# Kernel tuning notes

Hardware: AMD Instinct MI355X
Metric: run time of the kernel (lower is better)

Reference implementation:

```python
import jax, jax.numpy as jnp
import numpy as np

B, N, H, V, STEP = 16, 50, 128, 40000, 2

def setup_inputs() -> dict:
    key = jax.random.key(0)
    ks = jax.random.split(key, 24)
    def nrm(i, shape, s=0.08):
        return jax.random.normal(ks[i], shape, jnp.float32) * s
    items = jax.random.randint(ks[0], (B, N), 0, V)
    A = jax.random.uniform(ks[1], (B, N, 2 * N), jnp.float32)
    lengths = jax.random.randint(ks[2], (B,), 1, N + 1)
    mask = (jnp.arange(N)[None, :] < lengths[:, None]).astype(jnp.int32)
    emb = nrm(3, (V, H), 0.1).at[0].set(0.0)  # padding_idx=0 row zeroed
    return dict(
        items=items, A=A, mask=mask, emb=emb,
        w_ih=nrm(4, (3 * H, 2 * H)), w_hh=nrm(5, (3 * H, H)),
        b_ih=nrm(6, (3 * H,)), b_hh=nrm(7, (3 * H,)),
        b_iah=nrm(8, (H,)), b_oah=nrm(9, (H,)),
        W_ein=nrm(10, (H, H)), b_ein=nrm(11, (H,)),
        W_eout=nrm(12, (H, H)), b_eout=nrm(13, (H,)),
        W_one=nrm(14, (H, H)), b_one=nrm(15, (H,)),
        W_two=nrm(16, (H, H)), b_two=nrm(17, (H,)),
        w_three=nrm(18, (H,)),
        W_tr=nrm(19, (H, 2 * H)), b_tr=nrm(20, (H,)),
        W_t=nrm(21, (H, H)),
    )

def gnn_cell(A, hidden, w_ih, w_hh, b_ih, b_hh, b_iah, b_oah, W_ein, b_ein, W_eout, b_eout):
    # A: [B,N,2N], hidden: [B,N,H]
    ein = hidden @ W_ein.T + b_ein
    eout = hidden @ W_eout.T + b_eout
    input_in = jnp.einsum('bnm,bmh->bnh', A[:, :, :N], ein) + b_iah
    input_out = jnp.einsum('bnm,bmh->bnh', A[:, :, N:], eout) + b_oah
    inputs = jnp.concatenate([input_in, input_out], axis=-1)  # [B,N,2H]
    gi = inputs @ w_ih.T + b_ih
    gh = hidden @ w_hh.T + b_hh
    i_r, i_i, i_n = jnp.split(gi, 3, axis=-1)
    h_r, h_i, h_n = jnp.split(gh, 3, axis=-1)
    resetgate = jax.nn.sigmoid(i_r + h_r)
    inputgate = jax.nn.sigmoid(i_i + h_i)
    newgate = jnp.tanh(i_n + resetgate * h_n)
    return newgate + inputgate * (hidden - newgate)

def reference(items, A, mask, emb, w_ih, w_hh, b_ih, b_hh, b_iah, b_oah,
              W_ein, b_ein, W_eout, b_eout, W_one, b_one, W_two, b_two,
              w_three, W_tr, b_tr, W_t):
    hidden = emb[items]  # [B,N,H]
    for _ in range(STEP):
        hidden = gnn_cell(A, hidden, w_ih, w_hh, b_ih, b_hh, b_iah, b_oah,
                          W_ein, b_ein, W_eout, b_eout)
    # compute_scores
    lengths = jnp.sum(mask, axis=1)  # all >= 1 by construction
    ht = hidden[jnp.arange(B), lengths - 1]  # [B,H] last valid item
    q1 = (ht @ W_one.T + b_one)[:, None, :]
    q2 = hidden @ W_two.T + b_two
    mexp = mask[..., None].astype(jnp.float32)  # [B,N,1]
    alpha_logits = jax.nn.sigmoid(q1 + q2) @ w_three[:, None]  # [B,N,1]
    alpha = jax.nn.softmax(jnp.where(mexp == 0, -jnp.inf, alpha_logits), axis=1)
    a = jnp.sum(alpha * hidden * mexp, axis=1)  # [B,H]
    a = jnp.concatenate([a, ht], axis=1) @ W_tr.T + b_tr  # hybrid (nonhybrid=False)
    b_emb = emb[1:]  # [V-1,H]
    qt = (hidden * mexp) @ W_t.T  # [B,N,H]
    beta_logits = jnp.einsum('vh,bnh->bvn', b_emb, qt)
    beta_logits = jnp.where(mask[:, None, :] == 0, -jnp.inf, beta_logits)
    beta = jax.nn.softmax(beta_logits, axis=-1)  # [B,V-1,N]
    target = jnp.einsum('bvn,bnh->bvh', beta, qt * mexp)  # [B,V-1,H]
    # scores = sum((a[:,None,:] + target) * b_emb, -1), split to avoid extra buffer
    scores = jnp.einsum('bvh,vh->bv', target, b_emb) + a @ b_emb.T
    return scores  # [B, V-1]
```

## Files before the change

kernel.cpp:

```cpp
#include <hip/hip_runtime.h>

#define BB 16
#define NN 50
#define HH 128
#define VV 40000
#define VO 39999

typedef unsigned short u16;
typedef unsigned int u32;
typedef __attribute__((ext_vector_type(8))) short short8;
typedef __attribute__((ext_vector_type(4))) float f32x4;

#define OFF_HID    0
#define OFF_HID2   102400
#define OFF_Q2     102400
#define OFF_Q1     204800
#define OFF_HT     206848
#define OFF_QTBF   307200
#define OFF_LEN    411648
#define OFF_WIHT   411664
#define OFF_WHHT   509968
#define OFF_WEINT  559120
#define OFF_WEOUTT 575504
#define OFF_WTWOT  591888
#define OFF_WTT    608272
#define OFF_WONET  624656
#define OFF_WTRT   641040

__device__ __forceinline__ float sigm(float x){ return 1.0f/(1.0f+__expf(-x)); }
__device__ __forceinline__ float b2f(u16 u){
  union { u32 i; float f; } c; c.i = ((u32)u) << 16; return c.f;
}
__device__ __forceinline__ u16 f2b(float f){
  union { float f; u32 i; } c; c.f = f;
  u32 u = c.i;
  return (u16)((u + 0x7fffu + ((u >> 16) & 1u)) >> 16);
}
__device__ __forceinline__ int frag_idx(int b, int n, int k){
  int tile = n>>4, vlo = n&15, kc = k>>5, quad = (k>>3)&3, j = k&7;
  return (((b*4+tile)*4+kc)<<9) + ((quad<<4)+vlo)*8 + j;
}

__global__ void k_pre(const int* __restrict__ items, const float* __restrict__ emb,
                      const float* __restrict__ w_ih, const float* __restrict__ w_hh,
                      const float* __restrict__ W_ein, const float* __restrict__ W_eout,
                      const float* __restrict__ W_two, const float* __restrict__ W_t,
                      const float* __restrict__ W_one, const float* __restrict__ W_tr,
                      float* __restrict__ ws){
  int idx = blockIdx.x*256 + threadIdx.x;
  if (idx < 102400){
    int r = idx >> 7, h = idx & 127;
    ws[OFF_HID + idx] = emb[items[r]*128 + h];
  } else if (idx < 200704){
    int i = idx-102400; int k=i/384, j=i-k*384;
    ws[OFF_WIHT + i] = w_ih[j*256 + k];
  } else if (idx < 249856){
    int i = idx-200704; int k=i/384, j=i-k*384;
    ws[OFF_WHHT + i] = w_hh[j*128 + k];
  } else if (idx < 266240){
    int i = idx-249856; int k=i>>7, h=i&127;
    ws[OFF_WEINT + i] = W_ein[h*128 + k];
  } else if (idx < 282624){
    int i = idx-266240; int k=i>>7, h=i&127;
    ws[OFF_WEOUTT + i] = W_eout[h*128 + k];
  } else if (idx < 299008){
    int i = idx-282624; int k=i>>7, h=i&127;
    ws[OFF_WTWOT + i] = W_two[h*128 + k];
  } else if (idx < 315392){
    int i = idx-299008; int k=i>>7, h=i&127;
    ws[OFF_WTT + i] = W_t[h*128 + k];
  } else if (idx < 331776){
    int i = idx-315392; int k=i>>7, h=i&127;
    ws[OFF_WONET + i] = W_one[h*128 + k];
  } else if (idx < 364544){
    int i = idx-331776; int k=i>>7, h=i&127;
    ws[OFF_WTRT + i] = W_tr[h*256 + k];
  }
}

__global__ void __launch_bounds__(384) k_step(const float* __restrict__ A,
                       const float* __restrict__ b_ein, const float* __restrict__ b_eout,
                       const float* __restrict__ b_iah, const float* __restrict__ b_oah,
                       const float* __restrict__ b_ih, const float* __restrict__ b_hh,
                       float* __restrict__ ws, int srcOff, int dstOff){
  __shared__ float hall[52][128];
  __shared__ float arow[4][104];
  __shared__ float hAl[4][256];
  __shared__ float sAl[4][2];
  __shared__ float inp[4][256];
  __shared__ float gil[4][384];
  __shared__ float ghl[4][384];
  int t = threadIdx.x;
  int tile = blockIdx.x, b = blockIdx.y;
  int n0 = tile*4;
  const float* hsrc = ws + srcOff + b*6400;
  for (int o=t; o<6656; o+=384) hall[o>>7][o&127] = (o<6400) ? hsrc[o] : 0.0f;
  for (int o=t; o<416; o+=384){
    int r=o/104, c=o-r*104;
    arow[r][c] = (c<100 && n0+r<NN) ? A[(size_t)(b*NN+n0+r)*100 + c] : 0.0f;
  }
  __syncthreads();
  for (int o=t; o<1024; o+=384){
    int r = o>>8, kk = o&255;
    int k = kk & 127;
    const float* ar = &arow[r][(kk>>7)*50];
    float acc = 0.0f;
    #pragma unroll 5
    for (int m=0;m<50;m++) acc += ar[m]*hall[m][k];
    hAl[r][kk] = acc;
  }
  if (t < 8){
    int r = t>>1, half = t&1;
    const float* ar = &arow[r][half*50];
    float s = 0.0f;
    for (int m=0;m<50;m++) s += ar[m];
    sAl[r][half] = s;
  }
  __syncthreads();
  for (int o=t; o<1024; o+=384){
    int r = o>>8, c8 = o&255;
    int in_half = (c8 < 128);
    int c = c8 & 127;
    const float* wT = ws + (in_half ? OFF_WEINT : OFF_WEOUTT);
    const float* hv = &hAl[r][in_half ? 0 : 128];
    float acc = in_half ? (b_iah[c] + sAl[r][0]*b_ein[c])
                        : (b_oah[c] + sAl[r][1]*b_eout[c]);
    for (int k=0;k<128;k+=4){
      float4 h4 = *(const float4*)(hv + k);
      acc += h4.x*wT[(k+0)*128+c] + h4.y*wT[(k+1)*128+c]
           + h4.z*wT[(k+2)*128+c] + h4.w*wT[(k+3)*128+c];
    }
    inp[r][c8] = acc;
  }
  __syncthreads();
  {
    int j = t;
    float gi[4], gh[4];
    float bi2 = b_ih[j], bh2 = b_hh[j];
    #pragma unroll
    for (int r=0;r<4;r++){ gi[r]=bi2; gh[r]=bh2; }
    const float* wti = ws + OFF_WIHT;
    const float* wth = ws + OFF_WHHT;
    for (int k=0;k<256;k+=4){
      float w0 = wti[(k+0)*384+j], w1 = wti[(k+1)*384+j];
      float w2 = wti[(k+2)*384+j], w3_ = wti[(k+3)*384+j];
      #pragma unroll
      for (int r=0;r<4;r++){
        float4 iv = *(const float4*)(&inp[r][k]);
        gi[r] += iv.x*w0 + iv.y*w1 + iv.z*w2 + iv.w*w3_;
      }
    }
    for (int k=0;k<128;k+=4){
      float w0 = wth[(k+0)*384+j], w1 = wth[(k+1)*384+j];
      float w2 = wth[(k+2)*384+j], w3_ = wth[(k+3)*384+j];
      #pragma unroll
      for (int r=0;r<4;r++){
        float4 hv = *(const float4*)(&hall[n0+r][k]);
        gh[r] += hv.x*w0 + hv.y*w1 + hv.z*w2 + hv.w*w3_;
      }
    }
    #pragma unroll
    for (int r=0;r<4;r++){ gil[r][j]=gi[r]; ghl[r][j]=gh[r]; }
  }
  __syncthreads();
  for (int o=t; o<512; o+=384){
    int r=o>>7, h=o&127, row=n0+r;
    if (row<NN){
      float ir_=gil[r][h], ii=gil[r][128+h], inw=gil[r][256+h];
      float hr_=ghl[r][h], hi2=ghl[r][128+h], hn=ghl[r][256+h];
      float rg=sigm(ir_+hr_), ig=sigm(ii+hi2), ng=tanhf(inw+rg*hn);
      float hv=hall[n0+r][h];
      ws[dstOff + (b*NN+row)*128 + h] = ng + ig*(hv-ng);
    }
  }
}

__global__ void __launch_bounds__(256) k_post(const int* __restrict__ mask,
                      const float* __restrict__ b_two, const float* __restrict__ b_one,
                      float* __restrict__ ws){
  int bx = blockIdx.x, t = threadIdx.x;
  u16* qtbf = (u16*)(ws + OFF_QTBF);
  if (bx < 200){
    bool isq2 = bx < 100;
    int r0 = (isq2 ? bx : bx-100) * 8;
    __shared__ float hl[1024];
    for (int i=0;i<4;i++) hl[t+i*256] = ws[OFF_HID + r0*128 + t + i*256];
    __syncthreads();
    int h = t & 127, g = t >> 7;
    const float* wT = ws + (isq2 ? OFF_WTWOT : OFF_WTT);
    float binit = isq2 ? b_two[h] : 0.0f;
    float acc[4];
    #pragma unroll
    for (int r=0;r<4;r++) acc[r] = binit;
    for (int k4=0;k4<32;k4++){
      int k = k4*4;
      float w0 = wT[(k+0)*128+h], w1 = wT[(k+1)*128+h];
      float w2 = wT[(k+2)*128+h], w3 = wT[(k+3)*128+h];
      #pragma unroll
      for (int r=0;r<4;r++){
        float4 hv = *(const float4*)(hl + (g*4+r)*128 + k);
        acc[r] += hv.x*w0 + hv.y*w1 + hv.z*w2 + hv.w*w3;
      }
    }
    #pragma unroll
    for (int r=0;r<4;r++){
      int row = r0 + g*4 + r;
      if (isq2) ws[OFF_Q2 + row*128 + h] = acc[r];
      else {
        float val = mask[row] ? acc[r] : 0.0f;
        int b = row/NN, n = row - b*NN;
        qtbf[frag_idx(b, n, h)] = f2b(val);
      }
    }
  } else if (bx < 248){
    int i = (bx-200)*256 + t;
    #pragma unroll
    for (int kk=0;kk<2;kk++){
      int e = i*2 + kk;
      int b = e/1536, rem = e - b*1536;
      int kc = rem/384, rem2 = rem - kc*384;
      int quad = rem2/96, vv = rem2 - quad*96;
      int vlo = 4 + vv/8, j = vv & 7;
      qtbf[(((b*4+3)*4+kc)<<9) + ((quad<<4)+vlo)*8 + j] = 0;
    }
  } else {
    __shared__ float htl[128];
    int b = bx - 248;
    if (t < 128){
      int len = 0;
      for (int n=0;n<NN;n++) len += mask[b*NN+n];
      if (len<1) len=1; if (len>NN) len=NN;
      float ht = ws[OFF_HID + (b*NN + len-1)*128 + t];
      ws[OFF_HT + b*128 + t] = ht;
      htl[t] = ht;
      if (t==0) ((int*)(ws+OFF_LEN))[b] = len;
    }
    __syncthreads();
    if (t < 128){
      const float* w1T = ws + OFF_WONET;
      float q1 = b_one[t];
      for (int k=0;k<128;k+=4){
        float4 h4 = *(const float4*)(htl + k);
        q1 += h4.x*w1T[(k+0)*128+t] + h4.y*w1T[(k+1)*128+t]
            + h4.z*w1T[(k+2)*128+t] + h4.w*w1T[(k+3)*128+t];
      }
      ws[OFF_Q1 + b*128 + t] = q1;
    }
  }
}

__global__ void __launch_bounds__(256) k_attn2(const float* __restrict__ w_three,
                        const float* __restrict__ b_tr, float* __restrict__ ws){
  __shared__ float q2l[NN*129];
  __shared__ float q1l[128], w3l[128], htl[128], al[128], pt2[128], alg[64];
  int t = threadIdx.x;
  int b = blockIdx.x;
  for (int o=t;o<6400;o+=256){ int n=o>>7, h=o&127; q2l[n*129+h] = ws[OFF_Q2 + b*6400 + o]; }
  if (t < 128){
    q1l[t] = ws[OFF_Q1 + b*128 + t];
    w3l[t] = w_three[t];
    htl[t] = ws[OFF_HT + b*128 + t];
  }
  int len = ((const int*)(ws+OFF_LEN))[b];
  __syncthreads();
  if (t < 200){
    int n = t>>2, part = t&3;
    if (n < len){
      const float* qr  = q2l + n*129 + part*32;
      const float* q1p = q1l + part*32;
      const float* w3p = w3l + part*32;
      float s = 0.0f;
      for (int h=0;h<32;h++) s += w3p[h]*sigm(q1p[h]+qr[h]);
      s += __shfl_xor(s,1); s += __shfl_xor(s,2);
      if (part==0) alg[n] = s;
    }
  }
  __syncthreads();
  if (t < 64){
    float v = (t<len) ? alg[t] : -1e30f;
    float m = v;
    m = fmaxf(m, __shfl_xor(m,1));  m = fmaxf(m, __shfl_xor(m,2));
    m = fmaxf(m, __shfl_xor(m,4));  m = fmaxf(m, __shfl_xor(m,8));
    m = fmaxf(m, __shfl_xor(m,16)); m = fmaxf(m, __shfl_xor(m,32));
    float e = (t<len) ? __expf(v - m) : 0.0f;
    float ss = e;
    ss += __shfl_xor(ss,1);  ss += __shfl_xor(ss,2);
    ss += __shfl_xor(ss,4);  ss += __shfl_xor(ss,8);
    ss += __shfl_xor(ss,16); ss += __shfl_xor(ss,32);
    float inv = 1.0f/ss;
    if (t<len) alg[t] = e*inv;
  }
  __syncthreads();
  if (t < 128){
    const float* hid = ws + OFF_HID + b*6400;
    float a = 0.0f;
    for (int n=0;n<len;n++) a += alg[n]*hid[n*128+t];
    al[t] = a;
  }
  __syncthreads();
  float p1 = 0.0f;
  if (t < 256){
    int g2 = t>>7, h = t&127;
    const float* wtr = ws + OFF_WTRT + g2*128*128;
    const float* src = g2 ? htl : al;
    float p = 0.0f;
    for (int k=0;k<128;k++) p += src[k]*wtr[k*128+h];
    if (g2) pt2[h] = p; else p1 = p;
  }
  __syncthreads();
  if (t < 128){
    float af = b_tr[t] + p1 + pt2[t];
    u16 hi = f2b(af);
    u16 lo = f2b(af - b2f(hi));
    u16* qtbf = (u16*)(ws + OFF_QTBF);
    qtbf[frag_idx(b, 50, t)] = hi;
    qtbf[frag_idx(b, 51, t)] = lo;
  }
}

__global__ void __launch_bounds__(256) k_scores(const float* __restrict__ emb,
                                                const float* __restrict__ ws,
                                                float* __restrict__ out){
  __shared__ u16 qlds[8192];
  int tid = threadIdx.x;
  int lane = tid & 63, wave = tid >> 6;
  int quad = lane >> 4, vlo = lane & 15;
  int v = blockIdx.y*64 + wave*16 + vlo;
  int vc = (v < VO) ? v : (VO-1);
  const float* erow = emb + (size_t)(vc+1)*128;
  short8 bfr[4];
  #pragma unroll
  for (int kc=0;kc<4;kc++){
    const float4* p = (const float4*)(erow + kc*32 + quad*8);
    float4 x = p[0], y = p[1];
    union { short8 s; u32 w[4]; } u;
    u.w[0] = (u32)f2b(x.x) | ((u32)f2b(x.y)<<16);
    u.w[1] = (u32)f2b(x.z) | ((u32)f2b(x.w)<<16);
    u.w[2] = (u32)f2b(y.x) | ((u32)f2b(y.y)<<16);
    u.w[3] = (u32)f2b(y.z) | ((u32)f2b(y.w)<<16);
    bfr[kc] = u.s;
  }
  const u16* qtf = (const u16*)(ws + OFF_QTBF);
  const int* slen = (const int*)(ws + OFF_LEN);
  int b0 = blockIdx.x*4;
  for (int bi=0;bi<4;bi++){
    int b = b0 + bi;
    __syncthreads();
    {
      const uint4* src = (const uint4*)qtf + (size_t)b*1024;
      uint4* dst = (uint4*)qlds;
      #pragma unroll
      for (int r=0;r<4;r++) dst[tid + r*256] = src[tid + r*256];
    }
    __syncthreads();
    int len = slen[b];
    f32x4 acc0={0.f,0.f,0.f,0.f}, acc1=acc0, acc2=acc0, acc3=acc0;
    #pragma unroll
    for (int kc=0;kc<4;kc++){
      const u16* base = qlds + kc*512 + lane*8;
      short8 a0 = *(const short8*)(base + 0*2048);
      short8 a1 = *(const short8*)(base + 1*2048);
      short8 a2 = *(const short8*)(base + 2*2048);
      short8 a3 = *(const short8*)(base + 3*2048);
      acc0 = __builtin_amdgcn_mfma_f32_16x16x32_bf16(a0, bfr[kc], acc0, 0,0,0);
      acc1 = __builtin_amdgcn_mfma_f32_16x16x32_bf16(a1, bfr[kc], acc1, 0,0,0);
      acc2 = __builtin_amdgcn_mfma_f32_16x16x32_bf16(a2, bfr[kc], acc2, 0,0,0);
      acc3 = __builtin_amdgcn_mfma_f32_16x16x32_bf16(a3, bfr[kc], acc3, 0,0,0);
    }
    int nb = quad*4;
    float ss=0.f, nm=0.f;
    #pragma unroll
    for (int r=0;r<4;r++){
      { int n=nb+r;    if(n<len){ float e=__expf(acc0[r]); ss+=e; nm+=e*acc0[r]; } }
      { int n=nb+r+16; if(n<len){ float e=__expf(acc1[r]); ss+=e; nm+=e*acc1[r]; } }
      { int n=nb+r+32; if(n<len){ float e=__expf(acc2[r]); ss+=e; nm+=e*acc2[r]; } }
      { int n=nb+r+48; if(n<len){ float e=__expf(acc3[r]); ss+=e; nm+=e*acc3[r]; } }
    }
    ss += __shfl_xor(ss,16); ss += __shfl_xor(ss,32);
    nm += __shfl_xor(nm,16); nm += __shfl_xor(nm,32);
    if (quad==0 && v < VO){
      float pa = acc3[2] + acc3[3];
      out[(size_t)b*VO + v] = nm/ss + pa;
    }
  }
}

extern "C" void kernel_launch(void* const* d_in, const int* in_sizes, int n_in,
                              void* d_out, int out_size, void* d_ws, size_t ws_size,
                              hipStream_t stream){
  const int*   items  = (const int*)d_in[0];
  const float* A      = (const float*)d_in[1];
  const int*   mask   = (const int*)d_in[2];
  const float* emb    = (const float*)d_in[3];
  const float* w_ih   = (const float*)d_in[4];
  const float* w_hh   = (const float*)d_in[5];
  const float* b_ih   = (const float*)d_in[6];
  const float* b_hh   = (const float*)d_in[7];
  const float* b_iah  = (const float*)d_in[8];
  const float* b_oah  = (const float*)d_in[9];
  const float* W_ein  = (const float*)d_in[10];
  const float* b_ein  = (const float*)d_in[11];
  const float* W_eout = (const float*)d_in[12];
  const float* b_eout = (const float*)d_in[13];
  const float* W_one  = (const float*)d_in[14];
  const float* b_one  = (const float*)d_in[15];
  const float* W_two  = (const float*)d_in[16];
  const float* b_two  = (const float*)d_in[17];
  const float* w_three= (const float*)d_in[18];
  const float* W_tr   = (const float*)d_in[19];
  const float* b_tr   = (const float*)d_in[20];
  const float* W_t    = (const float*)d_in[21];
  float* ws  = (float*)d_ws;
  float* out = (float*)d_out;

  k_pre<<<1424,256,0,stream>>>(items,emb,w_ih,w_hh,W_ein,W_eout,W_two,W_t,W_one,W_tr,ws);
  k_step<<<dim3(13,16),384,0,stream>>>(A,b_ein,b_eout,b_iah,b_oah,b_ih,b_hh,ws,OFF_HID,OFF_HID2);
  k_step<<<dim3(13,16),384,0,stream>>>(A,b_ein,b_eout,b_iah,b_oah,b_ih,b_hh,ws,OFF_HID2,OFF_HID);
  k_post<<<264,256,0,stream>>>(mask,b_two,b_one,ws);
  k_attn2<<<16,256,0,stream>>>(w_three,b_tr,ws);
  k_scores<<<dim3(4,625),256,0,stream>>>(emb,ws,out);
}
```

Before: 213.9 us.

## Read GNN weights row-major directly and halve rows per k_step block

Removes the transposed copies of w_ih, w_hh, W_ein and W_eout from the preprocessing kernel. k_step now reads the original row-major weights with per-thread float4 loads along k. Each block handles 2 node rows instead of 4, so the grid grows from 13x16 to 25x16 blocks. The aim is to cut preprocessing work and raise parallelism in the recurrent step. The cost is that each thread now walks its own weight row, so adjacent threads are strided apart and loads are uncoalesced, and every weight is re-read by twice as many blocks.

```diff
diff --git a/kernel.cpp b/kernel.cpp
--- a/kernel.cpp
+++ b/kernel.cpp
@@ -18,10 +18,6 @@
 #define OFF_HT     206848
 #define OFF_QTBF   307200
 #define OFF_LEN    411648
-#define OFF_WIHT   411664
-#define OFF_WHHT   509968
-#define OFF_WEINT  559120
-#define OFF_WEOUTT 575504
 #define OFF_WTWOT  591888
 #define OFF_WTT    608272
 #define OFF_WONET  624656
@@ -42,8 +38,6 @@
 }
 
 __global__ void k_pre(const int* __restrict__ items, const float* __restrict__ emb,
-                      const float* __restrict__ w_ih, const float* __restrict__ w_hh,
-                      const float* __restrict__ W_ein, const float* __restrict__ W_eout,
                       const float* __restrict__ W_two, const float* __restrict__ W_t,
                       const float* __restrict__ W_one, const float* __restrict__ W_tr,
                       float* __restrict__ ws){
@@ -51,56 +45,46 @@
   if (idx < 102400){
     int r = idx >> 7, h = idx & 127;
     ws[OFF_HID + idx] = emb[items[r]*128 + h];
-  } else if (idx < 200704){
-    int i = idx-102400; int k=i/384, j=i-k*384;
-    ws[OFF_WIHT + i] = w_ih[j*256 + k];
-  } else if (idx < 249856){
-    int i = idx-200704; int k=i/384, j=i-k*384;
-    ws[OFF_WHHT + i] = w_hh[j*128 + k];
-  } else if (idx < 266240){
-    int i = idx-249856; int k=i>>7, h=i&127;
-    ws[OFF_WEINT + i] = W_ein[h*128 + k];
-  } else if (idx < 282624){
-    int i = idx-266240; int k=i>>7, h=i&127;
-    ws[OFF_WEOUTT + i] = W_eout[h*128 + k];
-  } else if (idx < 299008){
-    int i = idx-282624; int k=i>>7, h=i&127;
+  } else if (idx < 118784){
+    int i = idx-102400; int k=i>>7, h=i&127;
     ws[OFF_WTWOT + i] = W_two[h*128 + k];
-  } else if (idx < 315392){
-    int i = idx-299008; int k=i>>7, h=i&127;
+  } else if (idx < 135168){
+    int i = idx-118784; int k=i>>7, h=i&127;
     ws[OFF_WTT + i] = W_t[h*128 + k];
-  } else if (idx < 331776){
-    int i = idx-315392; int k=i>>7, h=i&127;
+  } else if (idx < 151552){
+    int i = idx-135168; int k=i>>7, h=i&127;
     ws[OFF_WONET + i] = W_one[h*128 + k];
-  } else if (idx < 364544){
-    int i = idx-331776; int k=i>>7, h=i&127;
+  } else if (idx < 184320){
+    int i = idx-151552; int k=i>>7, h=i&127;
     ws[OFF_WTRT + i] = W_tr[h*256 + k];
   }
 }
 
 __global__ void __launch_bounds__(384) k_step(const float* __restrict__ A,
+                       const float* __restrict__ w_ih, const float* __restrict__ w_hh,
+                       const float* __restrict__ W_ein, const float* __restrict__ W_eout,
                        const float* __restrict__ b_ein, const float* __restrict__ b_eout,
                        const float* __restrict__ b_iah, const float* __restrict__ b_oah,
                        const float* __restrict__ b_ih, const float* __restrict__ b_hh,
                        float* __restrict__ ws, int srcOff, int dstOff){
-  __shared__ float hall[52][128];
-  __shared__ float arow[4][104];
-  __shared__ float hAl[4][256];
-  __shared__ float sAl[4][2];
-  __shared__ float inp[4][256];
-  __shared__ float gil[4][384];
-  __shared__ float ghl[4][384];
+  __shared__ float hall[50][128];
+  __shared__ float arow[2][104];
+  __shared__ float hAl[2][256];
+  __shared__ float sAl[2][2];
+  __shared__ float inp[2][256];
+  __shared__ float gil[2][384];
+  __shared__ float ghl[2][384];
   int t = threadIdx.x;
   int tile = blockIdx.x, b = blockIdx.y;
-  int n0 = tile*4;
+  int n0 = tile*2;
   const float* hsrc = ws + srcOff + b*6400;
-  for (int o=t; o<6656; o+=384) hall[o>>7][o&127] = (o<6400) ? hsrc[o] : 0.0f;
-  for (int o=t; o<416; o+=384){
+  for (int o=t; o<1600; o+=384) ((float4*)hall)[o] = ((const float4*)hsrc)[o];
+  for (int o=t; o<208; o+=384){
     int r=o/104, c=o-r*104;
-    arow[r][c] = (c<100 && n0+r<NN) ? A[(size_t)(b*NN+n0+r)*100 + c] : 0.0f;
-  }
-  __syncthreads();
-  for (int o=t; o<1024; o+=384){
+    arow[r][c] = (c<100) ? A[(size_t)(b*NN+n0+r)*100 + c] : 0.0f;
+  }
+  __syncthreads();
+  for (int o=t; o<512; o+=384){
     int r = o>>8, kk = o&255;
     int k = kk & 127;
     const float* ar = &arow[r][(kk>>7)*50];
@@ -109,7 +93,7 @@
     for (int m=0;m<50;m++) acc += ar[m]*hall[m][k];
     hAl[r][kk] = acc;
   }
-  if (t < 8){
+  if (t < 4){
     int r = t>>1, half = t&1;
     const float* ar = &arow[r][half*50];
     float s = 0.0f;
@@ -117,61 +101,54 @@
     sAl[r][half] = s;
   }
   __syncthreads();
-  for (int o=t; o<1024; o+=384){
+  for (int o=t; o<512; o+=384){
     int r = o>>8, c8 = o&255;
     int in_half = (c8 < 128);
     int c = c8 & 127;
-    const float* wT = ws + (in_half ? OFF_WEINT : OFF_WEOUTT);
+    const float* wrow = (in_half ? W_ein : W_eout) + c*128;
     const float* hv = &hAl[r][in_half ? 0 : 128];
     float acc = in_half ? (b_iah[c] + sAl[r][0]*b_ein[c])
                         : (b_oah[c] + sAl[r][1]*b_eout[c]);
+    #pragma unroll 8
     for (int k=0;k<128;k+=4){
+      float4 w4 = *(const float4*)(wrow + k);
       float4 h4 = *(const float4*)(hv + k);
-      acc += h4.x*wT[(k+0)*128+c] + h4.y*wT[(k+1)*128+c]
-           + h4.z*wT[(k+2)*128+c] + h4.w*wT[(k+3)*128+c];
+      acc += h4.x*w4.x + h4.y*w4.y + h4.z*w4.z + h4.w*w4.w;
     }
     inp[r][c8] = acc;
   }
   __syncthreads();
   {
     int j = t;
-    float gi[4], gh[4];
-    float bi2 = b_ih[j], bh2 = b_hh[j];
-    #pragma unroll
-    for (int r=0;r<4;r++){ gi[r]=bi2; gh[r]=bh2; }
-    const float* wti = ws + OFF_WIHT;
-    const float* wth = ws + OFF_WHHT;
+    float gi0=b_ih[j], gi1=gi0, gh0=b_hh[j], gh1=gh0;
+    const float* wi = w_ih + j*256;
+    const float* wh = w_hh + j*128;
+    #pragma unroll 8
     for (int k=0;k<256;k+=4){
-      float w0 = wti[(k+0)*384+j], w1 = wti[(k+1)*384+j];
-      float w2 = wti[(k+2)*384+j], w3_ = wti[(k+3)*384+j];
-      #pragma unroll
-      for (int r=0;r<4;r++){
-        float4 iv = *(const float4*)(&inp[r][k]);
-        gi[r] += iv.x*w0 + iv.y*w1 + iv.z*w2 + iv.w*w3_;
-      }
-    }
+      float4 w4 = *(const float4*)(wi + k);
+      float4 i0 = *(const float4*)(&inp[0][k]);
+      float4 i1 = *(const float4*)(&inp[1][k]);
+      gi0 += i0.x*w4.x + i0.y*w4.y + i0.z*w4.z + i0.w*w4.w;
+      gi1 += i1.x*w4.x + i1.y*w4.y + i1.z*w4.z + i1.w*w4.w;
+    }
+    #pragma unroll 8
     for (int k=0;k<128;k+=4){
-      float w0 = wth[(k+0)*384+j], w1 = wth[(k+1)*384+j];
-      float w2 = wth[(k+2)*384+j], w3_ = wth[(k+3)*384+j];
-      #pragma unroll
-      for (int r=0;r<4;r++){
-        float4 hv = *(const float4*)(&hall[n0+r][k]);
-        gh[r] += hv.x*w0 + hv.y*w1 + hv.z*w2 + hv.w*w3_;
-      }
-    }
-    #pragma unroll
-    for (int r=0;r<4;r++){ gil[r][j]=gi[r]; ghl[r][j]=gh[r]; }
-  }
-  __syncthreads();
-  for (int o=t; o<512; o+=384){
-    int r=o>>7, h=o&127, row=n0+r;
-    if (row<NN){
-      float ir_=gil[r][h], ii=gil[r][128+h], inw=gil[r][256+h];
-      float hr_=ghl[r][h], hi2=ghl[r][128+h], hn=ghl[r][256+h];
-      float rg=sigm(ir_+hr_), ig=sigm(ii+hi2), ng=tanhf(inw+rg*hn);
-      float hv=hall[n0+r][h];
-      ws[dstOff + (b*NN+row)*128 + h] = ng + ig*(hv-ng);
-    }
+      float4 w4 = *(const float4*)(wh + k);
+      float4 h0 = *(const float4*)(&hall[n0][k]);
+      float4 h1 = *(const float4*)(&hall[n0+1][k]);
+      gh0 += h0.x*w4.x + h0.y*w4.y + h0.z*w4.z + h0.w*w4.w;
+      gh1 += h1.x*w4.x + h1.y*w4.y + h1.z*w4.z + h1.w*w4.w;
+    }
+    gil[0][j]=gi0; gil[1][j]=gi1; ghl[0][j]=gh0; ghl[1][j]=gh1;
+  }
+  __syncthreads();
+  if (t < 256){
+    int r=t>>7, h=t&127, row=n0+r;
+    float ir_=gil[r][h], ii=gil[r][128+h], inw=gil[r][256+h];
+    float hr_=ghl[r][h], hi2=ghl[r][128+h], hn=ghl[r][256+h];
+    float rg=sigm(ir_+hr_), ig=sigm(ii+hi2), ng=tanhf(inw+rg*hn);
+    float hv=hall[row][h];
+    ws[dstOff + (b*NN+row)*128 + h] = ng + ig*(hv-ng);
   }
 }
 
@@ -413,9 +390,9 @@
   float* ws  = (float*)d_ws;
   float* out = (float*)d_out;
 
-  k_pre<<<1424,256,0,stream>>>(items,emb,w_ih,w_hh,W_ein,W_eout,W_two,W_t,W_one,W_tr,ws);
-  k_step<<<dim3(13,16),384,0,stream>>>(A,b_ein,b_eout,b_iah,b_oah,b_ih,b_hh,ws,OFF_HID,OFF_HID2);
-  k_step<<<dim3(13,16),384,0,stream>>>(A,b_ein,b_eout,b_iah,b_oah,b_ih,b_hh,ws,OFF_HID2,OFF_HID);
+  k_pre<<<720,256,0,stream>>>(items,emb,W_two,W_t,W_one,W_tr,ws);
+  k_step<<<dim3(25,16),384,0,stream>>>(A,w_ih,w_hh,W_ein,W_eout,b_ein,b_eout,b_iah,b_oah,b_ih,b_hh,ws,OFF_HID,OFF_HID2);
+  k_step<<<dim3(25,16),384,0,stream>>>(A,w_ih,w_hh,W_ein,W_eout,b_ein,b_eout,b_iah,b_oah,b_ih,b_hh,ws,OFF_HID2,OFF_HID);
   k_post<<<264,256,0,stream>>>(mask,b_two,b_one,ws);
   k_attn2<<<16,256,0,stream>>>(w_three,b_tr,ws);
   k_scores<<<dim3(4,625),256,0,stream>>>(emb,ws,out);
```

New measurement: 261.9 us. +22.4%, slower.

## Process one node row per block in GNN step kernel

Applied to the files above, without the earlier changes.

The GNN step kernel now assigns a single node row per block, launching 50x16 blocks instead of 13x16 blocks that each handled four rows. This spreads the work over more CUs on a GPU with many compute units. In exchange, each block reloads the whole 50x128 hidden tile and re-reads the full weight matrices for only one row, so weight traffic grows about fourfold. The hidden tile load is also vectorised to float4.

```diff
diff --git a/kernel.cpp b/kernel.cpp
--- a/kernel.cpp
+++ b/kernel.cpp
@@ -78,100 +78,70 @@
   }
 }
 
-__global__ void __launch_bounds__(384) k_step(const float* __restrict__ A,
+__global__ void __launch_bounds__(384) k_step3(const float* __restrict__ A,
                        const float* __restrict__ b_ein, const float* __restrict__ b_eout,
                        const float* __restrict__ b_iah, const float* __restrict__ b_oah,
                        const float* __restrict__ b_ih, const float* __restrict__ b_hh,
                        float* __restrict__ ws, int srcOff, int dstOff){
-  __shared__ float hall[52][128];
-  __shared__ float arow[4][104];
-  __shared__ float hAl[4][256];
-  __shared__ float sAl[4][2];
-  __shared__ float inp[4][256];
-  __shared__ float gil[4][384];
-  __shared__ float ghl[4][384];
+  __shared__ float hall[50][128];
+  __shared__ float arow[100];
+  __shared__ float hAl[256];
+  __shared__ float sa[2];
+  __shared__ float inpL[256];
+  __shared__ float gil[384];
+  __shared__ float ghl[384];
   int t = threadIdx.x;
-  int tile = blockIdx.x, b = blockIdx.y;
-  int n0 = tile*4;
+  int row = blockIdx.x, b = blockIdx.y;
   const float* hsrc = ws + srcOff + b*6400;
-  for (int o=t; o<6656; o+=384) hall[o>>7][o&127] = (o<6400) ? hsrc[o] : 0.0f;
-  for (int o=t; o<416; o+=384){
-    int r=o/104, c=o-r*104;
-    arow[r][c] = (c<100 && n0+r<NN) ? A[(size_t)(b*NN+n0+r)*100 + c] : 0.0f;
-  }
-  __syncthreads();
-  for (int o=t; o<1024; o+=384){
-    int r = o>>8, kk = o&255;
-    int k = kk & 127;
-    const float* ar = &arow[r][(kk>>7)*50];
+  for (int o=t; o<1600; o+=384) ((float4*)hall)[o] = ((const float4*)hsrc)[o];
+  if (t < 100) arow[t] = A[(size_t)(b*NN+row)*100 + t];
+  __syncthreads();
+  if (t < 256){
+    int k = t & 127;
+    const float* ar = arow + (t>>7)*50;
     float acc = 0.0f;
     #pragma unroll 5
     for (int m=0;m<50;m++) acc += ar[m]*hall[m][k];
-    hAl[r][kk] = acc;
-  }
-  if (t < 8){
-    int r = t>>1, half = t&1;
-    const float* ar = &arow[r][half*50];
+    hAl[t] = acc;
+  } else if (t < 258){
+    const float* ar = arow + (t-256)*50;
     float s = 0.0f;
     for (int m=0;m<50;m++) s += ar[m];
-    sAl[r][half] = s;
-  }
-  __syncthreads();
-  for (int o=t; o<1024; o+=384){
-    int r = o>>8, c8 = o&255;
-    int in_half = (c8 < 128);
-    int c = c8 & 127;
-    const float* wT = ws + (in_half ? OFF_WEINT : OFF_WEOUTT);
-    const float* hv = &hAl[r][in_half ? 0 : 128];
-    float acc = in_half ? (b_iah[c] + sAl[r][0]*b_ein[c])
-                        : (b_oah[c] + sAl[r][1]*b_eout[c]);
-    for (int k=0;k<128;k+=4){
-      float4 h4 = *(const float4*)(hv + k);
-      acc += h4.x*wT[(k+0)*128+c] + h4.y*wT[(k+1)*128+c]
-           + h4.z*wT[(k+2)*128+c] + h4.w*wT[(k+3)*128+c];
-    }
-    inp[r][c8] = acc;
+    sa[t-256] = s;
+  }
+  __syncthreads();
+  if (t < 256){
+    int c = t & 127;
+    int ih = (t < 128) ? 1 : 0;
+    const float* wT = ws + (ih ? OFF_WEINT : OFF_WEOUTT) + c;
+    const float* hv = hAl + (ih ? 0 : 128);
+    float acc = ih ? (b_iah[c] + sa[0]*b_ein[c]) : (b_oah[c] + sa[1]*b_eout[c]);
+    #pragma unroll 8
+    for (int k=0;k<128;k++) acc += hv[k]*wT[k*128];
+    inpL[t] = acc;
   }
   __syncthreads();
   {
     int j = t;
-    float gi[4], gh[4];
-    float bi2 = b_ih[j], bh2 = b_hh[j];
-    #pragma unroll
-    for (int r=0;r<4;r++){ gi[r]=bi2; gh[r]=bh2; }
-    const float* wti = ws + OFF_WIHT;
-    const float* wth = ws + OFF_WHHT;
-    for (int k=0;k<256;k+=4){
-      float w0 = wti[(k+0)*384+j], w1 = wti[(k+1)*384+j];
-      float w2 = wti[(k+2)*384+j], w3_ = wti[(k+3)*384+j];
-      #pragma unroll
-      for (int r=0;r<4;r++){
-        float4 iv = *(const float4*)(&inp[r][k]);
-        gi[r] += iv.x*w0 + iv.y*w1 + iv.z*w2 + iv.w*w3_;
-      }
-    }
-    for (int k=0;k<128;k+=4){
-      float w0 = wth[(k+0)*384+j], w1 = wth[(k+1)*384+j];
-      float w2 = wth[(k+2)*384+j], w3_ = wth[(k+3)*384+j];
-      #pragma unroll
-      for (int r=0;r<4;r++){
-        float4 hv = *(const float4*)(&hall[n0+r][k]);
-        gh[r] += hv.x*w0 + hv.y*w1 + hv.z*w2 + hv.w*w3_;
-      }
-    }
-    #pragma unroll
-    for (int r=0;r<4;r++){ gil[r][j]=gi[r]; ghl[r][j]=gh[r]; }
-  }
-  __syncthreads();
-  for (int o=t; o<512; o+=384){
-    int r=o>>7, h=o&127, row=n0+r;
-    if (row<NN){
-      float ir_=gil[r][h], ii=gil[r][128+h], inw=gil[r][256+h];
-      float hr_=ghl[r][h], hi2=ghl[r][128+h], hn=ghl[r][256+h];
-      float rg=sigm(ir_+hr_), ig=sigm(ii+hi2), ng=tanhf(inw+rg*hn);
-      float hv=hall[n0+r][h];
-      ws[dstOff + (b*NN+row)*128 + h] = ng + ig*(hv-ng);
-    }
+    const float* wiT = ws + OFF_WIHT + j;
+    float g = b_ih[j];
+    #pragma unroll 8
+    for (int k=0;k<256;k++) g += inpL[k]*wiT[k*384];
+    gil[j] = g;
+    const float* whT = ws + OFF_WHHT + j;
+    const float* hr = hall[row];
+    float g2 = b_hh[j];
+    #pragma unroll 8
+    for (int k=0;k<128;k++) g2 += hr[k]*whT[k*384];
+    ghl[j] = g2;
+  }
+  __syncthreads();
+  if (t < 128){
+    float ir_=gil[t], ii=gil[128+t], inw=gil[256+t];
+    float hr_=ghl[t], hi2=ghl[128+t], hn=ghl[256+t];
+    float rg=sigm(ir_+hr_), ig=sigm(ii+hi2), ng=tanhf(inw+rg*hn);
+    float hv=hall[row][t];
+    ws[dstOff + (b*NN+row)*128 + t] = ng + ig*(hv-ng);
   }
 }
 
@@ -240,9 +210,9 @@
       const float* w1T = ws + OFF_WONET;
       float q1 = b_one[t];
       for (int k=0;k<128;k+=4){
-        float4 h4 = *(const float4*)(htl + k);
-        q1 += h4.x*w1T[(k+0)*128+t] + h4.y*w1T[(k+1)*128+t]
-            + h4.z*w1T[(k+2)*128+t] + h4.w*w1T[(k+3)*128+t];
+        float4 h4v = *(const float4*)(htl + k);
+        q1 += h4v.x*w1T[(k+0)*128+t] + h4v.y*w1T[(k+1)*128+t]
+            + h4v.z*w1T[(k+2)*128+t] + h4v.w*w1T[(k+3)*128+t];
       }
       ws[OFF_Q1 + b*128 + t] = q1;
     }
@@ -414,9 +384,9 @@
   float* out = (float*)d_out;
 
   k_pre<<<1424,256,0,stream>>>(items,emb,w_ih,w_hh,W_ein,W_eout,W_two,W_t,W_one,W_tr,ws);
-  k_step<<<dim3(13,16),384,0,stream>>>(A,b_ein,b_eout,b_iah,b_oah,b_ih,b_hh,ws,OFF_HID,OFF_HID2);
-  k_step<<<dim3(13,16),384,0,stream>>>(A,b_ein,b_eout,b_iah,b_oah,b_ih,b_hh,ws,OFF_HID2,OFF_HID);
-  k_post<<<264,256,0,stream>>>(mask,b_two,b_one,ws);
+  k_step3<<<dim3(50,16),384,0,stream>>>(A,b_ein,b_eout,b_iah,b_oah,b_ih,b_hh,ws,OFF_HID,OFF_HID2);
+  k_step3<<<dim3(50,16),384,0,stream>>>(A,b_ein,b_eout,b_iah,b_oah,b_ih,b_hh,ws,OFF_HID2,OFF_HID);
+  k_post <<<264,256,0,stream>>>(mask,b_two,b_one,ws);
   k_attn2<<<16,256,0,stream>>>(w_three,b_tr,ws);
   k_scores<<<dim3(4,625),256,0,stream>>>(emb,ws,out);
 }
```

Result: slower. 219.1 us (+2.4%).
